# Optimization experiments

Measured on AMD Instinct MI355X. Metric: run time of the kernel, lower is better.

The kernel has to match this reference:

```python
import jax, jax.numpy as jnp
import numpy as np

E, D, P, T = 65536, 256, 4, 9
N_TYPES, N_SRC = 14, 4
# base-type order: nmos, pmos, balun, resistor, capacitor, inductor, vsource, isource, port
N_PARAMS = np.array([2, 2, 1, 1, 1, 1, 3, 2, 4], dtype=np.int32)
_S = np.ones((T, P), dtype=np.float32)
_S[0, 1] = 1e-6   # nmos w
_S[1, 1] = 1e-6   # pmos w
_S[3, 0] = 1e3    # resistor r
_S[4, 0] = 1e-12  # capacitor c
_S[5, 0] = 1e-9   # inductor l
_S[7, 0] = 1e-3   # isource dc
_S[7, 1] = 1e-3   # isource mag
_S[8, 2] = 1e9    # port freq
SCALES = jnp.asarray(_S)


def setup_inputs() -> dict:
    key = jax.random.key(0)
    ks = jax.random.split(key, 12)
    base_ids = jax.random.randint(ks[0], (E,), 0, T)
    type_ids = jax.random.randint(ks[1], (E,), 0, N_TYPES)
    source_ids = jax.random.randint(ks[2], (E,), 0, N_SRC)
    # raw params at physically realistic magnitude (pre-division values ~ scale)
    params = jax.random.uniform(ks[3], (E, P), jnp.float32) * SCALES[base_ids]
    W1 = jax.random.normal(ks[4], (T, P, D), jnp.float32) * 0.1
    # zero weight rows beyond each expert's param arity (matches torch pad/truncate)
    arity_mask = (np.arange(P)[None, :] < N_PARAMS[:, None]).astype(np.float32)
    W1 = W1 * jnp.asarray(arity_mask)[:, :, None]
    b1 = jax.random.normal(ks[5], (T, D), jnp.float32) * 0.1
    W2 = jax.random.normal(ks[6], (T, D, D), jnp.float32) * 0.05
    b2 = jax.random.normal(ks[7], (T, D), jnp.float32) * 0.05
    Wf = jax.random.normal(ks[8], (3 * D, D), jnp.float32) * 0.05
    bf = jax.random.normal(ks[9], (D,), jnp.float32) * 0.05
    type_embed = jax.random.normal(ks[10], (N_TYPES, D), jnp.float32)
    source_embed = jax.random.normal(ks[11], (N_SRC, D), jnp.float32)
    return {"type_ids": type_ids, "source_ids": source_ids, "base_ids": base_ids,
            "params": params, "type_embed": type_embed, "source_embed": source_embed,
            "W1": W1, "b1": b1, "W2": W2, "b2": b2, "Wf": Wf, "bf": bf}


def reference(type_ids, source_ids, base_ids, params, type_embed, source_embed,
              W1, b1, W2, b2, Wf, bf):
    # per-edge scale division (SCALE_FACTORS)
    x = params / SCALES[base_ids]                       # [E, P]
    # expert layer 1: gather tiny [P,D] weights per edge
    h = jax.nn.relu(jnp.einsum('ep,epd->ed', x, W1[base_ids]) + b1[base_ids])  # [E, D]
    # expert layer 2: masked per-type GEMMs (T is small/fixed)
    pv = jnp.zeros_like(h)
    for t in range(T):
        pv = jnp.where((base_ids == t)[:, None], h @ W2[t] + b2[t], pv)
    concat = jnp.concatenate([type_embed[type_ids], source_embed[source_ids], pv], axis=-1)  # [E, 3D]
    return jax.nn.relu(concat @ Wf + bf)                # [E, D]
```

## Files before the change

kernel.cpp:

```cpp
#include <hip/hip_runtime.h>

#define E_N 65536
#define T_N 9

typedef __bf16 bf16x8 __attribute__((ext_vector_type(8)));
typedef float f32x4 __attribute__((ext_vector_type(4)));
typedef unsigned short ushort8 __attribute__((ext_vector_type(8)));
union U8 { ushort8 u; bf16x8 b; };

#define OFF_CB   0
#define OFF_ABC  294912
#define OFF_D2   309248
#define OFF_BH   311552
#define OFF_CNT  313856
#define OFF_IDX  313872
#define WS_NEED_BYTES ((size_t)(313872 + 589824) * 4)

__device__ __constant__ float SCALES_C[9][4] = {
  {1.f,    1e-6f, 1.f,  1.f},
  {1.f,    1e-6f, 1.f,  1.f},
  {1.f,    1.f,   1.f,  1.f},
  {1e3f,   1.f,   1.f,  1.f},
  {1e-12f, 1.f,   1.f,  1.f},
  {1e-9f,  1.f,   1.f,  1.f},
  {1.f,    1.f,   1.f,  1.f},
  {1e-3f,  1e-3f, 1.f,  1.f},
  {1.f,    1.f,   1e9f, 1.f},
};

__device__ inline unsigned short f2bf(float f) {
  unsigned int u = __float_as_uint(f);
  unsigned int r = (u + 0x7FFFu + ((u >> 16) & 1u)) >> 16;
  return (unsigned short)r;
}

__global__ __launch_bounds__(256) void k_hist_embed(
    const int* __restrict__ base_ids,
    const float* __restrict__ te, const float* __restrict__ se,
    const float* __restrict__ b2, const float* __restrict__ Wf,
    const float* __restrict__ bfv,
    int* __restrict__ bh, float* __restrict__ ABc, float* __restrict__ D2b) {
  int b = blockIdx.x;
  int tid = threadIdx.x;

  if (b < 256) {
    __shared__ int ph[9][4];
    int e = (b << 8) + tid;
    int bt = base_ids[e];
    int w = tid >> 6, lane = tid & 63;
    #pragma unroll 1
    for (int t = 0; t < T_N; ++t) {
      unsigned long long m = __ballot(bt == t);
      if (lane == 0) ph[t][w] = __popcll(m);
    }
    __syncthreads();
    if (tid < T_N)
      bh[(tid << 8) + b] = ph[tid][0] + ph[tid][1] + ph[tid][2] + ph[tid][3];
  } else {
    int bb = b - 256, d = tid;
    if (bb < 56) {
      int ty = bb >> 2, sr = bb & 3;
      const float* t0 = te + ty * 256;
      const float* s0 = se + sr * 256;
      float a0 = 0.f, a1 = 0.f, a2 = 0.f, a3 = 0.f;
      #pragma unroll 4
      for (int k = 0; k < 256; k += 4) {
        a0 = fmaf(t0[k + 0], Wf[((k + 0) << 8) + d], a0);
        a1 = fmaf(t0[k + 1], Wf[((k + 1) << 8) + d], a1);
        a2 = fmaf(t0[k + 2], Wf[((k + 2) << 8) + d], a2);
        a3 = fmaf(t0[k + 3], Wf[((k + 3) << 8) + d], a3);
      }
      #pragma unroll 4
      for (int k = 0; k < 256; k += 4) {
        a0 = fmaf(s0[k + 0], Wf[((256 + k + 0) << 8) + d], a0);
        a1 = fmaf(s0[k + 1], Wf[((256 + k + 1) << 8) + d], a1);
        a2 = fmaf(s0[k + 2], Wf[((256 + k + 2) << 8) + d], a2);
        a3 = fmaf(s0[k + 3], Wf[((256 + k + 3) << 8) + d], a3);
      }
      ABc[(bb << 8) + d] = (a0 + a1) + (a2 + a3);
    } else {
      int t = bb - 56;
      const float* bp = b2 + t * 256;
      float a0 = bfv[d], a1 = 0.f, a2 = 0.f, a3 = 0.f;
      #pragma unroll 4
      for (int k = 0; k < 256; k += 4) {
        a0 = fmaf(bp[k + 0], Wf[((512 + k + 0) << 8) + d], a0);
        a1 = fmaf(bp[k + 1], Wf[((512 + k + 1) << 8) + d], a1);
        a2 = fmaf(bp[k + 2], Wf[((512 + k + 2) << 8) + d], a2);
        a3 = fmaf(bp[k + 3], Wf[((512 + k + 3) << 8) + d], a3);
      }
      D2b[(t << 8) + d] = (a0 + a1) + (a2 + a3);
    }
  }
}

__global__ __launch_bounds__(256) void k_c_scatter(
    const float* __restrict__ W2, const float* __restrict__ Wf,
    const int* __restrict__ base_ids, const int* __restrict__ type_ids,
    const int* __restrict__ source_ids, const int* __restrict__ bh,
    unsigned short* __restrict__ Cb, int* __restrict__ idx,
    int* __restrict__ cnt) {
  int b = blockIdx.x;
  int tid = threadIdx.x;

  if (b < 288) {
    int t = b >> 5;
    int j0 = (b & 31) << 3;
    __shared__ float w2s[8][256];
    for (int i = tid; i < 2048; i += 256)
      w2s[i >> 8][i & 255] = W2[t * 65536 + (j0 + (i >> 8)) * 256 + (i & 255)];
    __syncthreads();
    int dg = (tid & 63) << 2;
    int jg = (tid >> 6) << 1;
    f32x4 acc0 = {0.f, 0.f, 0.f, 0.f}, acc1 = {0.f, 0.f, 0.f, 0.f};
    #pragma unroll 4
    for (int k = 0; k < 256; ++k) {
      f32x4 wv = *(const f32x4*)&Wf[((512 + k) << 8) + dg];
      float a0 = w2s[jg][k], a1 = w2s[jg + 1][k];
      acc0.x = fmaf(a0, wv.x, acc0.x); acc0.y = fmaf(a0, wv.y, acc0.y);
      acc0.z = fmaf(a0, wv.z, acc0.z); acc0.w = fmaf(a0, wv.w, acc0.w);
      acc1.x = fmaf(a1, wv.x, acc1.x); acc1.y = fmaf(a1, wv.y, acc1.y);
      acc1.z = fmaf(a1, wv.z, acc1.z); acc1.w = fmaf(a1, wv.w, acc1.w);
    }
    unsigned short* CbT = Cb + (size_t)t * 65536;
    int j = j0 + jg;
    #pragma unroll
    for (int c = 0; c < 4; ++c) {
      int d = dg + c;
      unsigned int pk = (unsigned int)f2bf((c == 0) ? acc0.x : (c == 1) ? acc0.y : (c == 2) ? acc0.z : acc0.w)
                      | ((unsigned int)f2bf((c == 0) ? acc1.x : (c == 1) ? acc1.y : (c == 2) ? acc1.z : acc1.w) << 16);
      *(unsigned int*)&CbT[(((j >> 3) << 8) + d) * 8 + (j & 7)] = pk;
    }
  } else {
    int g = b - 288;
    int w = tid >> 6, lane = tid & 63;
    __shared__ int sph[9][4];
    __shared__ int redw[9][4];
    __shared__ int sbase[9];

    int e = (g << 8) + tid;
    int bt = base_ids[e];
    int pk = e | (type_ids[e] << 16) | (source_ids[e] << 20);
    unsigned long long lanebit = 1ull << lane;

    #pragma unroll 1
    for (int t = 0; t < T_N; ++t) {
      unsigned long long m = __ballot(bt == t);
      if (lane == 0) sph[t][w] = __popcll(m);
    }

    int v[9];
    #pragma unroll
    for (int t = 0; t < T_N; ++t) v[t] = (tid < g) ? bh[(t << 8) + tid] : 0;
    #pragma unroll
    for (int off = 32; off >= 1; off >>= 1) {
      #pragma unroll
      for (int t = 0; t < T_N; ++t) v[t] += __shfl_xor(v[t], off, 64);
    }
    if (lane == 0) {
      #pragma unroll
      for (int t = 0; t < T_N; ++t) redw[t][w] = v[t];
    }
    __syncthreads();
    if (tid < T_N) {
      sbase[tid] = redw[tid][0] + redw[tid][1] + redw[tid][2] + redw[tid][3];
      int tot = sph[tid][0] + sph[tid][1] + sph[tid][2] + sph[tid][3];
      if (g == 255) cnt[tid] = sbase[tid] + tot;
      int o = 0;
      #pragma unroll
      for (int ww = 0; ww < 4; ++ww) { int tmp = sph[tid][ww]; sph[tid][ww] = o; o += tmp; }
    }
    __syncthreads();

    #pragma unroll 1
    for (int t = 0; t < T_N; ++t) {
      unsigned long long m = __ballot(bt == t);
      if (bt == t) {
        int pos = sbase[t] + sph[t][w] + __popcll(m & (lanebit - 1ull));
        idx[t * E_N + pos] = pk;
      }
    }
  }
}

__global__ __launch_bounds__(256, 4) void edge_gemm(
    const int* __restrict__ cnt, const int* __restrict__ idxArr,
    const float* __restrict__ params,
    const float* __restrict__ W1, const float* __restrict__ b1,
    const unsigned short* __restrict__ Cb, const float* __restrict__ ABc,
    const float* __restrict__ D2b, float* __restrict__ out) {
  int b = blockIdx.x;
  int t = -1, m0 = 0, n = 0;
  {
    int acc = 0;
    #pragma unroll
    for (int tt = 0; tt < T_N; ++tt) {
      int c = cnt[tt];
      int nb = (c + 63) >> 6;
      if (t < 0 && b < acc + nb) { t = tt; m0 = (b - acc) << 6; n = c; }
      acc += nb;
    }
  }
  if (t < 0) return;

  __shared__ unsigned short hb[64 * 256];
  __shared__ int eidx[64];
  __shared__ float4 xs[64];

  int tid = threadIdx.x;
  if (tid < 64) {
    int m = m0 + tid;
    int mc = (m < n) ? m : (n - 1);
    int pk = idxArr[(size_t)t * E_N + mc];
    eidx[tid] = pk;
    int e = pk & 0xFFFF;
    float4 pr = *(const float4*)(params + (size_t)e * 4);
    float4 x;
    x.x = pr.x / SCALES_C[t][0];
    x.y = pr.y / SCALES_C[t][1];
    x.z = pr.z / SCALES_C[t][2];
    x.w = pr.w / SCALES_C[t][3];
    xs[tid] = x;
  }
  __syncthreads();

  {
    int d = tid;
    const float* W1t = W1 + t * 1024;
    float w0 = W1t[d], w1 = W1t[256 + d], w2 = W1t[512 + d], w3 = W1t[768 + d];
    float b1d = b1[t * 256 + d];
    int dbyte = d << 1;
    #pragma unroll 4
    for (int m = 0; m < 64; ++m) {
      float4 x = xs[m];
      float h = fmaf(x.x, w0, fmaf(x.y, w1, fmaf(x.z, w2, fmaf(x.w, w3, b1d))));
      h = fmaxf(h, 0.f);
      int off = (m << 9) + (dbyte ^ ((m & 7) << 4));
      hb[off >> 1] = f2bf(h);
    }
  }
  __syncthreads();

  int lane = tid & 63;
  int w = tid >> 6;
  int l15 = lane & 15;
  int l4 = lane >> 4;

  f32x4 acc[4][4];
  #pragma unroll
  for (int i = 0; i < 4; ++i)
    #pragma unroll
    for (int j = 0; j < 4; ++j) acc[i][j] = (f32x4){0.f, 0.f, 0.f, 0.f};

  const unsigned short* CbT = Cb + (size_t)t * 65536;

  #pragma unroll 1
  for (int s = 0; s < 8; ++s) {
    bf16x8 bfr[4];
    #pragma unroll
    for (int nn = 0; nn < 4; ++nn) {
      int koct = (s << 2) + l4;
      int d = (w << 6) + (nn << 4) + l15;
      U8 u;
      u.u = *(const ushort8*)(CbT + (size_t)((koct << 8) + d) * 8);
      bfr[nn] = u.b;
    }
    __builtin_amdgcn_s_setprio(1);
    #pragma unroll
    for (int mt = 0; mt < 4; ++mt) {
      int row = (mt << 4) + l15;
      int byte = (row << 9) + ((((s << 6) + (l4 << 4))) ^ ((row & 7) << 4));
      U8 a;
      a.u = *(const ushort8*)((const char*)hb + byte);
      #pragma unroll
      for (int nn = 0; nn < 4; ++nn)
        acc[mt][nn] = __builtin_amdgcn_mfma_f32_16x16x32_bf16(a.b, bfr[nn], acc[mt][nn], 0, 0, 0);
    }
    __builtin_amdgcn_s_setprio(0);
  }

  float* fb = (float*)hb;
  const float* d2p = D2b + (t << 8);
  #pragma unroll
  for (int p = 0; p < 2; ++p) {
    __syncthreads();
    #pragma unroll
    for (int mh = 0; mh < 2; ++mh) {
      int mt = (p << 1) + mh;
      int lrb = (mh << 4) + (l4 << 2);
      #pragma unroll
      for (int nn = 0; nn < 4; ++nn) {
        int col = (w << 6) + (nn << 4) + l15;
        #pragma unroll
        for (int r = 0; r < 4; ++r) {
          int lr = lrb + r;
          fb[lr * 256 + (col ^ ((lr & 7) << 2))] = acc[mt][nn][r];
        }
      }
    }
    __syncthreads();
    int lr = tid >> 3;
    int c8 = tid & 7;
    int row_g = (p << 5) + lr;
    if (m0 + row_g < n) {
      int pk = eidx[row_g];
      int e = pk & 0xFFFF;
      int ty = (pk >> 16) & 15;
      int sr = (pk >> 20) & 3;
      const float* abp = ABc + (size_t)(((ty << 2) + sr) << 8);
      float* op = out + (size_t)e * 256;
      int sw = (lr & 7) << 2;
      #pragma unroll
      for (int v = 0; v < 8; ++v) {
        int col = (c8 << 2) + (v << 5);
        f32x4 vv = *(const f32x4*)&fb[lr * 256 + (col ^ sw)];
        f32x4 ab = *(const f32x4*)&abp[col];
        f32x4 d2 = *(const f32x4*)&d2p[col];
        f32x4 rr;
        rr.x = fmaxf(vv.x + ab.x + d2.x, 0.f);
        rr.y = fmaxf(vv.y + ab.y + d2.y, 0.f);
        rr.z = fmaxf(vv.z + ab.z + d2.z, 0.f);
        rr.w = fmaxf(vv.w + ab.w + d2.w, 0.f);
        *(f32x4*)&op[col] = rr;
      }
    }
  }
}

extern "C" void kernel_launch(void* const* d_in, const int* in_sizes, int n_in,
                              void* d_out, int out_size, void* d_ws, size_t ws_size,
                              hipStream_t stream) {
  const int*   type_ids   = (const int*)  d_in[0];
  const int*   source_ids = (const int*)  d_in[1];
  const int*   base_ids   = (const int*)  d_in[2];
  const float* params     = (const float*)d_in[3];
  const float* type_embed = (const float*)d_in[4];
  const float* src_embed  = (const float*)d_in[5];
  const float* W1         = (const float*)d_in[6];
  const float* b1         = (const float*)d_in[7];
  const float* W2         = (const float*)d_in[8];
  const float* b2         = (const float*)d_in[9];
  const float* Wf         = (const float*)d_in[10];
  const float* bfv        = (const float*)d_in[11];
  float* out = (float*)d_out;

  if (ws_size < WS_NEED_BYTES) return;

  float* wsf = (float*)d_ws;
  unsigned short* Cb = (unsigned short*)(wsf + OFF_CB);
  float* ABc = wsf + OFF_ABC;
  float* D2b = wsf + OFF_D2;
  int*   bh  = (int*)(wsf + OFF_BH);
  int*   cnt = (int*)(wsf + OFF_CNT);
  int*   idx = (int*)(wsf + OFF_IDX);

  k_hist_embed<<<321, 256, 0, stream>>>(base_ids, type_embed, src_embed, b2, Wf,
                                        bfv, bh, ABc, D2b);
  k_c_scatter<<<544, 256, 0, stream>>>(W2, Wf, base_ids, type_ids, source_ids,
                                       bh, Cb, idx, cnt);
  edge_gemm<<<1033, 256, 0, stream>>>(cnt, idx, params, W1, b1, Cb, ABc, D2b, out);
}
```

Before: 66.37 us.

## Fuse prep and edge GEMM into one persistent cooperative kernel with grid sync

Replaces the three-kernel pipeline with a histogram kernel followed by one persistent cooperative kernel. That kernel runs the scatter, the embedding/bias projections and the W2·Wf product as work items in a grid-stride loop, then does a grid-wide sync and runs the edge GEMM tiles. Separately, the W2·Wf product is restructured so each block computes 8 rows with a K split across waves and an LDS reduction. The layer-1 h computation now processes two columns per thread with packed bf16 stores. The aim is to cut launch gaps and tail idle time between stages, at the cost of grid-sync overhead, more LDS through a union, and a persistent grid that may load-balance the GEMM tiles less well.

```diff
diff --git a/kernel.cpp b/kernel.cpp
--- a/kernel.cpp
+++ b/kernel.cpp
@@ -1,4 +1,7 @@
 #include <hip/hip_runtime.h>
+#include <hip/hip_cooperative_groups.h>
+
+namespace cg = cooperative_groups;
 
 #define E_N 65536
 #define T_N 9
@@ -7,6 +10,7 @@
 typedef float f32x4 __attribute__((ext_vector_type(4)));
 typedef unsigned short ushort8 __attribute__((ext_vector_type(8)));
 union U8 { ushort8 u; bf16x8 b; };
+union BF2 { __bf16 h[2]; unsigned int u; };
 
 #define OFF_CB   0
 #define OFF_ABC  294912
@@ -34,294 +38,344 @@
   return (unsigned short)r;
 }
 
-__global__ __launch_bounds__(256) void k_hist_embed(
-    const int* __restrict__ base_ids,
+struct GemmSM {
+  unsigned short hb[64 * 256];
+  int eidx[64];
+  float4 xs[64];
+};
+struct CSM {
+  float w2s[8][256];
+  float partf[3 * 64 * 32];
+};
+struct ScatSM {
+  int sph[9][4];
+  int redw[9][4];
+  int sbase[9];
+};
+union SM { GemmSM g; CSM c; ScatSM s; };
+
+__global__ __launch_bounds__(256) void k_hist(const int* __restrict__ base_ids,
+                                              int* __restrict__ bh) {
+  __shared__ int ph[9][4];
+  int b = blockIdx.x, tid = threadIdx.x;
+  int e = (b << 8) + tid;
+  int bt = base_ids[e];
+  int w = tid >> 6, lane = tid & 63;
+  #pragma unroll 1
+  for (int t = 0; t < T_N; ++t) {
+    unsigned long long m = __ballot(bt == t);
+    if (lane == 0) ph[t][w] = __popcll(m);
+  }
+  __syncthreads();
+  if (tid < T_N)
+    bh[(tid << 8) + b] = ph[tid][0] + ph[tid][1] + ph[tid][2] + ph[tid][3];
+}
+
+__global__ __launch_bounds__(256, 4) void fused(
+    int phase,
+    const int* __restrict__ base_ids, const int* __restrict__ type_ids,
+    const int* __restrict__ source_ids, const float* __restrict__ params,
     const float* __restrict__ te, const float* __restrict__ se,
-    const float* __restrict__ b2, const float* __restrict__ Wf,
-    const float* __restrict__ bfv,
-    int* __restrict__ bh, float* __restrict__ ABc, float* __restrict__ D2b) {
-  int b = blockIdx.x;
+    const float* __restrict__ W1, const float* __restrict__ b1,
+    const float* __restrict__ W2, const float* __restrict__ b2,
+    const float* __restrict__ Wf, const float* __restrict__ bfv,
+    const int* __restrict__ bh,
+    int* cnt, int* idxArr, unsigned short* Cb,
+    float* ABc, float* D2b, float* out) {
+  __shared__ SM sm;
   int tid = threadIdx.x;
-
-  if (b < 256) {
-    __shared__ int ph[9][4];
-    int e = (b << 8) + tid;
-    int bt = base_ids[e];
-    int w = tid >> 6, lane = tid & 63;
-    #pragma unroll 1
-    for (int t = 0; t < T_N; ++t) {
-      unsigned long long m = __ballot(bt == t);
-      if (lane == 0) ph[t][w] = __popcll(m);
-    }
-    __syncthreads();
-    if (tid < T_N)
-      bh[(tid << 8) + b] = ph[tid][0] + ph[tid][1] + ph[tid][2] + ph[tid][3];
-  } else {
-    int bb = b - 256, d = tid;
-    if (bb < 56) {
-      int ty = bb >> 2, sr = bb & 3;
-      const float* t0 = te + ty * 256;
-      const float* s0 = se + sr * 256;
-      float a0 = 0.f, a1 = 0.f, a2 = 0.f, a3 = 0.f;
-      #pragma unroll 4
-      for (int k = 0; k < 256; k += 4) {
-        a0 = fmaf(t0[k + 0], Wf[((k + 0) << 8) + d], a0);
-        a1 = fmaf(t0[k + 1], Wf[((k + 1) << 8) + d], a1);
-        a2 = fmaf(t0[k + 2], Wf[((k + 2) << 8) + d], a2);
-        a3 = fmaf(t0[k + 3], Wf[((k + 3) << 8) + d], a3);
-      }
-      #pragma unroll 4
-      for (int k = 0; k < 256; k += 4) {
-        a0 = fmaf(s0[k + 0], Wf[((256 + k + 0) << 8) + d], a0);
-        a1 = fmaf(s0[k + 1], Wf[((256 + k + 1) << 8) + d], a1);
-        a2 = fmaf(s0[k + 2], Wf[((256 + k + 2) << 8) + d], a2);
-        a3 = fmaf(s0[k + 3], Wf[((256 + k + 3) << 8) + d], a3);
-      }
-      ABc[(bb << 8) + d] = (a0 + a1) + (a2 + a3);
-    } else {
-      int t = bb - 56;
-      const float* bp = b2 + t * 256;
-      float a0 = bfv[d], a1 = 0.f, a2 = 0.f, a3 = 0.f;
-      #pragma unroll 4
-      for (int k = 0; k < 256; k += 4) {
-        a0 = fmaf(bp[k + 0], Wf[((512 + k + 0) << 8) + d], a0);
-        a1 = fmaf(bp[k + 1], Wf[((512 + k + 1) << 8) + d], a1);
-        a2 = fmaf(bp[k + 2], Wf[((512 + k + 2) << 8) + d], a2);
-        a3 = fmaf(bp[k + 3], Wf[((512 + k + 3) << 8) + d], a3);
-      }
-      D2b[(t << 8) + d] = (a0 + a1) + (a2 + a3);
-    }
-  }
-}
-
-__global__ __launch_bounds__(256) void k_c_scatter(
-    const float* __restrict__ W2, const float* __restrict__ Wf,
-    const int* __restrict__ base_ids, const int* __restrict__ type_ids,
-    const int* __restrict__ source_ids, const int* __restrict__ bh,
-    unsigned short* __restrict__ Cb, int* __restrict__ idx,
-    int* __restrict__ cnt) {
-  int b = blockIdx.x;
-  int tid = threadIdx.x;
-
-  if (b < 288) {
-    int t = b >> 5;
-    int j0 = (b & 31) << 3;
-    __shared__ float w2s[8][256];
-    for (int i = tid; i < 2048; i += 256)
-      w2s[i >> 8][i & 255] = W2[t * 65536 + (j0 + (i >> 8)) * 256 + (i & 255)];
-    __syncthreads();
-    int dg = (tid & 63) << 2;
-    int jg = (tid >> 6) << 1;
-    f32x4 acc0 = {0.f, 0.f, 0.f, 0.f}, acc1 = {0.f, 0.f, 0.f, 0.f};
-    #pragma unroll 4
-    for (int k = 0; k < 256; ++k) {
-      f32x4 wv = *(const f32x4*)&Wf[((512 + k) << 8) + dg];
-      float a0 = w2s[jg][k], a1 = w2s[jg + 1][k];
-      acc0.x = fmaf(a0, wv.x, acc0.x); acc0.y = fmaf(a0, wv.y, acc0.y);
-      acc0.z = fmaf(a0, wv.z, acc0.z); acc0.w = fmaf(a0, wv.w, acc0.w);
-      acc1.x = fmaf(a1, wv.x, acc1.x); acc1.y = fmaf(a1, wv.y, acc1.y);
-      acc1.z = fmaf(a1, wv.z, acc1.z); acc1.w = fmaf(a1, wv.w, acc1.w);
-    }
-    unsigned short* CbT = Cb + (size_t)t * 65536;
-    int j = j0 + jg;
-    #pragma unroll
-    for (int c = 0; c < 4; ++c) {
-      int d = dg + c;
-      unsigned int pk = (unsigned int)f2bf((c == 0) ? acc0.x : (c == 1) ? acc0.y : (c == 2) ? acc0.z : acc0.w)
-                      | ((unsigned int)f2bf((c == 0) ? acc1.x : (c == 1) ? acc1.y : (c == 2) ? acc1.z : acc1.w) << 16);
-      *(unsigned int*)&CbT[(((j >> 3) << 8) + d) * 8 + (j & 7)] = pk;
-    }
-  } else {
-    int g = b - 288;
-    int w = tid >> 6, lane = tid & 63;
-    __shared__ int sph[9][4];
-    __shared__ int redw[9][4];
-    __shared__ int sbase[9];
-
-    int e = (g << 8) + tid;
-    int bt = base_ids[e];
-    int pk = e | (type_ids[e] << 16) | (source_ids[e] << 20);
-    unsigned long long lanebit = 1ull << lane;
-
-    #pragma unroll 1
-    for (int t = 0; t < T_N; ++t) {
-      unsigned long long m = __ballot(bt == t);
-      if (lane == 0) sph[t][w] = __popcll(m);
-    }
-
-    int v[9];
-    #pragma unroll
-    for (int t = 0; t < T_N; ++t) v[t] = (tid < g) ? bh[(t << 8) + tid] : 0;
-    #pragma unroll
-    for (int off = 32; off >= 1; off >>= 1) {
-      #pragma unroll
-      for (int t = 0; t < T_N; ++t) v[t] += __shfl_xor(v[t], off, 64);
-    }
-    if (lane == 0) {
-      #pragma unroll
-      for (int t = 0; t < T_N; ++t) redw[t][w] = v[t];
-    }
-    __syncthreads();
-    if (tid < T_N) {
-      sbase[tid] = redw[tid][0] + redw[tid][1] + redw[tid][2] + redw[tid][3];
-      int tot = sph[tid][0] + sph[tid][1] + sph[tid][2] + sph[tid][3];
-      if (g == 255) cnt[tid] = sbase[tid] + tot;
-      int o = 0;
-      #pragma unroll
-      for (int ww = 0; ww < 4; ++ww) { int tmp = sph[tid][ww]; sph[tid][ww] = o; o += tmp; }
-    }
-    __syncthreads();
-
-    #pragma unroll 1
-    for (int t = 0; t < T_N; ++t) {
-      unsigned long long m = __ballot(bt == t);
-      if (bt == t) {
-        int pos = sbase[t] + sph[t][w] + __popcll(m & (lanebit - 1ull));
-        idx[t * E_N + pos] = pk;
-      }
-    }
-  }
-}
-
-__global__ __launch_bounds__(256, 4) void edge_gemm(
-    const int* __restrict__ cnt, const int* __restrict__ idxArr,
-    const float* __restrict__ params,
-    const float* __restrict__ W1, const float* __restrict__ b1,
-    const unsigned short* __restrict__ Cb, const float* __restrict__ ABc,
-    const float* __restrict__ D2b, float* __restrict__ out) {
-  int b = blockIdx.x;
-  int t = -1, m0 = 0, n = 0;
-  {
-    int acc = 0;
-    #pragma unroll
-    for (int tt = 0; tt < T_N; ++tt) {
-      int c = cnt[tt];
-      int nb = (c + 63) >> 6;
-      if (t < 0 && b < acc + nb) { t = tt; m0 = (b - acc) << 6; n = c; }
-      acc += nb;
-    }
-  }
-  if (t < 0) return;
-
-  __shared__ unsigned short hb[64 * 256];
-  __shared__ int eidx[64];
-  __shared__ float4 xs[64];
-
-  int tid = threadIdx.x;
-  if (tid < 64) {
-    int m = m0 + tid;
-    int mc = (m < n) ? m : (n - 1);
-    int pk = idxArr[(size_t)t * E_N + mc];
-    eidx[tid] = pk;
-    int e = pk & 0xFFFF;
-    float4 pr = *(const float4*)(params + (size_t)e * 4);
-    float4 x;
-    x.x = pr.x / SCALES_C[t][0];
-    x.y = pr.y / SCALES_C[t][1];
-    x.z = pr.z / SCALES_C[t][2];
-    x.w = pr.w / SCALES_C[t][3];
-    xs[tid] = x;
-  }
-  __syncthreads();
-
-  {
-    int d = tid;
-    const float* W1t = W1 + t * 1024;
-    float w0 = W1t[d], w1 = W1t[256 + d], w2 = W1t[512 + d], w3 = W1t[768 + d];
-    float b1d = b1[t * 256 + d];
-    int dbyte = d << 1;
-    #pragma unroll 4
-    for (int m = 0; m < 64; ++m) {
-      float4 x = xs[m];
-      float h = fmaf(x.x, w0, fmaf(x.y, w1, fmaf(x.z, w2, fmaf(x.w, w3, b1d))));
-      h = fmaxf(h, 0.f);
-      int off = (m << 9) + (dbyte ^ ((m & 7) << 4));
-      hb[off >> 1] = f2bf(h);
-    }
-  }
-  __syncthreads();
-
+  int nb = gridDim.x;
   int lane = tid & 63;
   int w = tid >> 6;
-  int l15 = lane & 15;
-  int l4 = lane >> 4;
-
-  f32x4 acc[4][4];
-  #pragma unroll
-  for (int i = 0; i < 4; ++i)
+
+  if (phase <= 1) {
+    for (int it = blockIdx.x; it < 609; it += nb) {
+      if (it < 256) {
+        int g = it;
+        int e = (g << 8) + tid;
+        int bt = base_ids[e];
+        int pk = e | (type_ids[e] << 16) | (source_ids[e] << 20);
+        unsigned long long lanebit = 1ull << lane;
+
+        #pragma unroll 1
+        for (int t = 0; t < T_N; ++t) {
+          unsigned long long m = __ballot(bt == t);
+          if (lane == 0) sm.s.sph[t][w] = __popcll(m);
+        }
+        int v[9];
+        #pragma unroll
+        for (int t = 0; t < T_N; ++t) v[t] = (tid < g) ? bh[(t << 8) + tid] : 0;
+        #pragma unroll
+        for (int off = 32; off >= 1; off >>= 1) {
+          #pragma unroll
+          for (int t = 0; t < T_N; ++t) v[t] += __shfl_xor(v[t], off, 64);
+        }
+        if (lane == 0) {
+          #pragma unroll
+          for (int t = 0; t < T_N; ++t) sm.s.redw[t][w] = v[t];
+        }
+        __syncthreads();
+        if (tid < T_N) {
+          sm.s.sbase[tid] = sm.s.redw[tid][0] + sm.s.redw[tid][1] +
+                            sm.s.redw[tid][2] + sm.s.redw[tid][3];
+          int tot = sm.s.sph[tid][0] + sm.s.sph[tid][1] +
+                    sm.s.sph[tid][2] + sm.s.sph[tid][3];
+          if (g == 255) cnt[tid] = sm.s.sbase[tid] + tot;
+          int o = 0;
+          #pragma unroll
+          for (int ww = 0; ww < 4; ++ww) {
+            int tmp = sm.s.sph[tid][ww]; sm.s.sph[tid][ww] = o; o += tmp;
+          }
+        }
+        __syncthreads();
+        #pragma unroll 1
+        for (int t = 0; t < T_N; ++t) {
+          unsigned long long m = __ballot(bt == t);
+          if (bt == t) {
+            int pos = sm.s.sbase[t] + sm.s.sph[t][w] + __popcll(m & (lanebit - 1ull));
+            idxArr[t * E_N + pos] = pk;
+          }
+        }
+      } else if (it < 321) {
+        int bb = it - 256, d = tid;
+        if (bb < 56) {
+          int ty = bb >> 2, sr = bb & 3;
+          const float* t0 = te + ty * 256;
+          const float* s0 = se + sr * 256;
+          float a0 = 0.f, a1 = 0.f, a2 = 0.f, a3 = 0.f;
+          #pragma unroll 4
+          for (int k = 0; k < 256; k += 4) {
+            a0 = fmaf(t0[k + 0], Wf[((k + 0) << 8) + d], a0);
+            a1 = fmaf(t0[k + 1], Wf[((k + 1) << 8) + d], a1);
+            a2 = fmaf(t0[k + 2], Wf[((k + 2) << 8) + d], a2);
+            a3 = fmaf(t0[k + 3], Wf[((k + 3) << 8) + d], a3);
+          }
+          #pragma unroll 4
+          for (int k = 0; k < 256; k += 4) {
+            a0 = fmaf(s0[k + 0], Wf[((256 + k + 0) << 8) + d], a0);
+            a1 = fmaf(s0[k + 1], Wf[((256 + k + 1) << 8) + d], a1);
+            a2 = fmaf(s0[k + 2], Wf[((256 + k + 2) << 8) + d], a2);
+            a3 = fmaf(s0[k + 3], Wf[((256 + k + 3) << 8) + d], a3);
+          }
+          ABc[(bb << 8) + d] = (a0 + a1) + (a2 + a3);
+        } else {
+          int t = bb - 56;
+          const float* bp = b2 + t * 256;
+          float a0 = bfv[d], a1 = 0.f, a2 = 0.f, a3 = 0.f;
+          #pragma unroll 4
+          for (int k = 0; k < 256; k += 4) {
+            a0 = fmaf(bp[k + 0], Wf[((512 + k + 0) << 8) + d], a0);
+            a1 = fmaf(bp[k + 1], Wf[((512 + k + 1) << 8) + d], a1);
+            a2 = fmaf(bp[k + 2], Wf[((512 + k + 2) << 8) + d], a2);
+            a3 = fmaf(bp[k + 3], Wf[((512 + k + 3) << 8) + d], a3);
+          }
+          D2b[(t << 8) + d] = (a0 + a1) + (a2 + a3);
+        }
+      } else {
+        int ci = it - 321;
+        int t = ci >> 5;
+        int j0 = (ci & 31) << 3;
+        for (int i = tid; i < 2048; i += 256)
+          sm.c.w2s[i >> 8][i & 255] =
+              W2[(size_t)t * 65536 + (size_t)(j0 + (i >> 8)) * 256 + (i & 255)];
+        __syncthreads();
+
+        int dg = lane << 2;
+        int kbase = w << 6;
+        f32x4 acc[8];
+        #pragma unroll
+        for (int j = 0; j < 8; ++j) acc[j] = (f32x4){0.f, 0.f, 0.f, 0.f};
+        #pragma unroll 2
+        for (int k0 = 0; k0 < 64; k0 += 4) {
+          f32x4 a[8];
+          #pragma unroll
+          for (int j = 0; j < 8; ++j) a[j] = *(const f32x4*)&sm.c.w2s[j][kbase + k0];
+          #pragma unroll
+          for (int kk = 0; kk < 4; ++kk) {
+            f32x4 wv = *(const f32x4*)&Wf[((512 + kbase + k0 + kk) << 8) + dg];
+            #pragma unroll
+            for (int j = 0; j < 8; ++j) {
+              float aj = a[j][kk];
+              acc[j].x = fmaf(aj, wv.x, acc[j].x);
+              acc[j].y = fmaf(aj, wv.y, acc[j].y);
+              acc[j].z = fmaf(aj, wv.z, acc[j].z);
+              acc[j].w = fmaf(aj, wv.w, acc[j].w);
+            }
+          }
+        }
+        if (w > 0) {
+          int fb = (((w - 1) << 6) + lane) << 5;
+          #pragma unroll
+          for (int j = 0; j < 8; ++j)
+            *(f32x4*)&sm.c.partf[fb + ((j ^ (lane & 7)) << 2)] = acc[j];
+        }
+        __syncthreads();
+        if (w == 0) {
+          #pragma unroll
+          for (int p = 0; p < 3; ++p) {
+            int fb = ((p << 6) + lane) << 5;
+            #pragma unroll
+            for (int j = 0; j < 8; ++j)
+              acc[j] += *(const f32x4*)&sm.c.partf[fb + ((j ^ (lane & 7)) << 2)];
+          }
+          unsigned short* CbT = Cb + (size_t)t * 65536;
+          #pragma unroll
+          for (int di = 0; di < 4; ++di) {
+            ushort8 o;
+            #pragma unroll
+            for (int j = 0; j < 8; ++j) o[j] = f2bf(acc[j][di]);
+            *(ushort8*)(CbT + ((size_t)((j0 >> 3) << 8) + dg + di) * 8) = o;
+          }
+        }
+      }
+      __syncthreads();
+    }
+  }
+
+  if (phase < 0) {
+    __threadfence();
+    cg::this_grid().sync();
+  }
+
+  if (phase < 0 || phase == 2) {
+    int tcnt[9];
     #pragma unroll
-    for (int j = 0; j < 4; ++j) acc[i][j] = (f32x4){0.f, 0.f, 0.f, 0.f};
-
-  const unsigned short* CbT = Cb + (size_t)t * 65536;
-
-  #pragma unroll 1
-  for (int s = 0; s < 8; ++s) {
-    bf16x8 bfr[4];
+    for (int i2 = 0; i2 < 9; ++i2) tcnt[i2] = cnt[i2];
+    int tot = 0;
     #pragma unroll
-    for (int nn = 0; nn < 4; ++nn) {
-      int koct = (s << 2) + l4;
-      int d = (w << 6) + (nn << 4) + l15;
-      U8 u;
-      u.u = *(const ushort8*)(CbT + (size_t)((koct << 8) + d) * 8);
-      bfr[nn] = u.b;
-    }
-    __builtin_amdgcn_s_setprio(1);
-    #pragma unroll
-    for (int mt = 0; mt < 4; ++mt) {
-      int row = (mt << 4) + l15;
-      int byte = (row << 9) + ((((s << 6) + (l4 << 4))) ^ ((row & 7) << 4));
-      U8 a;
-      a.u = *(const ushort8*)((const char*)hb + byte);
+    for (int i2 = 0; i2 < 9; ++i2) tot += (tcnt[i2] + 63) >> 6;
+
+    for (int tile = blockIdx.x; tile < tot; tile += nb) {
+      __syncthreads();
+      int t = 0, m0 = 0, accb = 0;
       #pragma unroll
-      for (int nn = 0; nn < 4; ++nn)
-        acc[mt][nn] = __builtin_amdgcn_mfma_f32_16x16x32_bf16(a.b, bfr[nn], acc[mt][nn], 0, 0, 0);
-    }
-    __builtin_amdgcn_s_setprio(0);
-  }
-
-  float* fb = (float*)hb;
-  const float* d2p = D2b + (t << 8);
-  #pragma unroll
-  for (int p = 0; p < 2; ++p) {
-    __syncthreads();
-    #pragma unroll
-    for (int mh = 0; mh < 2; ++mh) {
-      int mt = (p << 1) + mh;
-      int lrb = (mh << 4) + (l4 << 2);
+      for (int tt = 0; tt < T_N; ++tt) {
+        int nbk = (tcnt[tt] + 63) >> 6;
+        if (tile >= accb && tile < accb + nbk) { t = tt; m0 = (tile - accb) << 6; }
+        accb += nbk;
+      }
+      int n = tcnt[t];
+
+      if (tid < 64) {
+        int m = m0 + tid;
+        int mc = (m < n) ? m : (n - 1);
+        int pk = idxArr[(size_t)t * E_N + mc];
+        sm.g.eidx[tid] = pk;
+        int e = pk & 0xFFFF;
+        float4 pr = *(const float4*)(params + (size_t)e * 4);
+        float4 x;
+        x.x = pr.x / SCALES_C[t][0];
+        x.y = pr.y / SCALES_C[t][1];
+        x.z = pr.z / SCALES_C[t][2];
+        x.w = pr.w / SCALES_C[t][3];
+        sm.g.xs[tid] = x;
+      }
+      __syncthreads();
+
+      {
+        int dp = tid & 127, mh = tid >> 7;
+        int d0 = dp << 1;
+        const float* W1t = W1 + t * 1024;
+        float2 wq0 = *(const float2*)&W1t[d0];
+        float2 wq1 = *(const float2*)&W1t[256 + d0];
+        float2 wq2 = *(const float2*)&W1t[512 + d0];
+        float2 wq3 = *(const float2*)&W1t[768 + d0];
+        float2 bq  = *(const float2*)&b1[t * 256 + d0];
+        int mb = mh << 5;
+        #pragma unroll 4
+        for (int i = 0; i < 32; ++i) {
+          int m = mb + i;
+          float4 x = sm.g.xs[m];
+          float h0 = fmaf(x.x, wq0.x, fmaf(x.y, wq1.x, fmaf(x.z, wq2.x, fmaf(x.w, wq3.x, bq.x))));
+          float h1 = fmaf(x.x, wq0.y, fmaf(x.y, wq1.y, fmaf(x.z, wq2.y, fmaf(x.w, wq3.y, bq.y))));
+          BF2 pk2;
+          pk2.h[0] = (__bf16)fmaxf(h0, 0.f);
+          pk2.h[1] = (__bf16)fmaxf(h1, 0.f);
+          int off = (m << 9) + ((d0 << 1) ^ ((m & 7) << 4));
+          *(unsigned int*)((char*)sm.g.hb + off) = pk2.u;
+        }
+      }
+      __syncthreads();
+
+      int l15 = lane & 15;
+      int l4 = lane >> 4;
+      f32x4 acc[4][4];
       #pragma unroll
-      for (int nn = 0; nn < 4; ++nn) {
-        int col = (w << 6) + (nn << 4) + l15;
-        #pragma unroll
-        for (int r = 0; r < 4; ++r) {
-          int lr = lrb + r;
-          fb[lr * 256 + (col ^ ((lr & 7) << 2))] = acc[mt][nn][r];
-        }
-      }
-    }
-    __syncthreads();
-    int lr = tid >> 3;
-    int c8 = tid & 7;
-    int row_g = (p << 5) + lr;
-    if (m0 + row_g < n) {
-      int pk = eidx[row_g];
-      int e = pk & 0xFFFF;
-      int ty = (pk >> 16) & 15;
-      int sr = (pk >> 20) & 3;
-      const float* abp = ABc + (size_t)(((ty << 2) + sr) << 8);
-      float* op = out + (size_t)e * 256;
-      int sw = (lr & 7) << 2;
+      for (int i = 0; i < 4; ++i)
+        #pragma unroll
+        for (int j = 0; j < 4; ++j) acc[i][j] = (f32x4){0.f, 0.f, 0.f, 0.f};
+
+      const unsigned short* CbT = Cb + (size_t)t * 65536;
+      #pragma unroll 1
+      for (int s = 0; s < 8; ++s) {
+        bf16x8 bfr[4];
+        #pragma unroll
+        for (int nn = 0; nn < 4; ++nn) {
+          int koct = (s << 2) + l4;
+          int d = (w << 6) + (nn << 4) + l15;
+          U8 u;
+          u.u = *(const ushort8*)(CbT + (size_t)((koct << 8) + d) * 8);
+          bfr[nn] = u.b;
+        }
+        __builtin_amdgcn_s_setprio(1);
+        #pragma unroll
+        for (int mt = 0; mt < 4; ++mt) {
+          int row = (mt << 4) + l15;
+          int byte = (row << 9) + ((((s << 6) + (l4 << 4))) ^ ((row & 7) << 4));
+          U8 a;
+          a.u = *(const ushort8*)((const char*)sm.g.hb + byte);
+          #pragma unroll
+          for (int nn = 0; nn < 4; ++nn)
+            acc[mt][nn] = __builtin_amdgcn_mfma_f32_16x16x32_bf16(a.b, bfr[nn], acc[mt][nn], 0, 0, 0);
+        }
+        __builtin_amdgcn_s_setprio(0);
+      }
+
+      float* fb = (float*)sm.g.hb;
+      const float* d2p = D2b + (t << 8);
       #pragma unroll
-      for (int v = 0; v < 8; ++v) {
-        int col = (c8 << 2) + (v << 5);
-        f32x4 vv = *(const f32x4*)&fb[lr * 256 + (col ^ sw)];
-        f32x4 ab = *(const f32x4*)&abp[col];
-        f32x4 d2 = *(const f32x4*)&d2p[col];
-        f32x4 rr;
-        rr.x = fmaxf(vv.x + ab.x + d2.x, 0.f);
-        rr.y = fmaxf(vv.y + ab.y + d2.y, 0.f);
-        rr.z = fmaxf(vv.z + ab.z + d2.z, 0.f);
-        rr.w = fmaxf(vv.w + ab.w + d2.w, 0.f);
-        *(f32x4*)&op[col] = rr;
+      for (int p = 0; p < 2; ++p) {
+        __syncthreads();
+        #pragma unroll
+        for (int mh2 = 0; mh2 < 2; ++mh2) {
+          int mt = (p << 1) + mh2;
+          int lrb = (mh2 << 4) + (l4 << 2);
+          #pragma unroll
+          for (int nn = 0; nn < 4; ++nn) {
+            int col = (w << 6) + (nn << 4) + l15;
+            #pragma unroll
+            for (int r = 0; r < 4; ++r) {
+              int lr = lrb + r;
+              fb[lr * 256 + (col ^ ((lr & 7) << 2))] = acc[mt][nn][r];
+            }
+          }
+        }
+        __syncthreads();
+        int lr = tid >> 3;
+        int c8 = tid & 7;
+        int row_g = (p << 5) + lr;
+        if (m0 + row_g < n) {
+          int pk = sm.g.eidx[row_g];
+          int e = pk & 0xFFFF;
+          int ty = (pk >> 16) & 15;
+          int sr = (pk >> 20) & 3;
+          const float* abp = ABc + (size_t)(((ty << 2) + sr) << 8);
+          float* op = out + (size_t)e * 256;
+          int sw = (lr & 7) << 2;
+          #pragma unroll
+          for (int vv2 = 0; vv2 < 8; ++vv2) {
+            int col = (c8 << 2) + (vv2 << 5);
+            f32x4 vvv = *(const f32x4*)&fb[lr * 256 + (col ^ sw)];
+            f32x4 ab = *(const f32x4*)&abp[col];
+            f32x4 d2 = *(const f32x4*)&d2p[col];
+            f32x4 rr;
+            rr.x = fmaxf(vvv.x + ab.x + d2.x, 0.f);
+            rr.y = fmaxf(vvv.y + ab.y + d2.y, 0.f);
+            rr.z = fmaxf(vvv.z + ab.z + d2.z, 0.f);
+            rr.w = fmaxf(vvv.w + ab.w + d2.w, 0.f);
+            *(f32x4*)&op[col] = rr;
+          }
+        }
       }
     }
   }
@@ -334,8 +388,8 @@
   const int*   source_ids = (const int*)  d_in[1];
   const int*   base_ids   = (const int*)  d_in[2];
   const float* params     = (const float*)d_in[3];
-  const float* type_embed = (const float*)d_in[4];
-  const float* src_embed  = (const float*)d_in[5];
+  const float* te         = (const float*)d_in[4];
+  const float* se         = (const float*)d_in[5];
   const float* W1         = (const float*)d_in[6];
   const float* b1         = (const float*)d_in[7];
   const float* W2         = (const float*)d_in[8];
@@ -354,9 +408,35 @@
   int*   cnt = (int*)(wsf + OFF_CNT);
   int*   idx = (int*)(wsf + OFF_IDX);
 
-  k_hist_embed<<<321, 256, 0, stream>>>(base_ids, type_embed, src_embed, b2, Wf,
-                                        bfv, bh, ABc, D2b);
-  k_c_scatter<<<544, 256, 0, stream>>>(W2, Wf, base_ids, type_ids, source_ids,
-                                       bh, Cb, idx, cnt);
-  edge_gemm<<<1033, 256, 0, stream>>>(cnt, idx, params, W1, b1, Cb, ABc, D2b, out);
+  k_hist<<<256, 256, 0, stream>>>(base_ids, bh);
+
+  int maxb = 0;
+  hipError_t oe = hipOccupancyMaxActiveBlocksPerMultiprocessor(
+      &maxb, (const void*)fused, 256, 0);
+  int grid = (oe == hipSuccess && maxb > 0) ? maxb * 256 : 0;
+  if (grid > 1024) grid = 1024;
+  bool coop = (grid >= 256);
+
+  if (coop) {
+    int ph = -1;
+    void* args[] = {(void*)&ph,
+                    (void*)&base_ids, (void*)&type_ids, (void*)&source_ids,
+                    (void*)&params,   (void*)&te,       (void*)&se,
+                    (void*)&W1,       (void*)&b1,       (void*)&W2,
+                    (void*)&b2,       (void*)&Wf,       (void*)&bfv,
+                    (void*)&bh,       (void*)&cnt,      (void*)&idx,
+                    (void*)&Cb,       (void*)&ABc,      (void*)&D2b,
+                    (void*)&out};
+    hipError_t le = hipLaunchCooperativeKernel((const void*)fused, dim3(grid),
+                                               dim3(256), args, 0, stream);
+    if (le != hipSuccess) coop = false;
+  }
+  if (!coop) {
+    fused<<<609, 256, 0, stream>>>(1, base_ids, type_ids, source_ids, params,
+                                   te, se, W1, b1, W2, b2, Wf, bfv, bh, cnt,
+                                   idx, Cb, ABc, D2b, out);
+    fused<<<1033, 256, 0, stream>>>(2, base_ids, type_ids, source_ids, params,
+                                    te, se, W1, b1, W2, b2, Wf, bfv, bh, cnt,
+                                    idx, Cb, ABc, D2b, out);
+  }
 }
```

Result: slower. 198.2 us (+198.6%).

## Fuse histogram, scatter and weight precompute into one prep kernel using atomics

Applied to the files above, without the earlier changes.

Merges the two preprocessing kernels into a single launch. Each block now claims its bucket offset with an atomicAdd on a per-type counter instead of the two-pass histogram plus prefix sum, and the counter is zeroed with a memset. The embedding and C-matrix precompute blocks are rewritten to split K across the four waves with vectorized float4 loads and a shared-memory reduction, and C now packs 8 outputs per store. This removes a kernel launch and the serial dependency on the histogram. The cost is that edge order within each type bucket is no longer deterministic, plus an extra memset node.

```diff
diff --git a/kernel.cpp b/kernel.cpp
--- a/kernel.cpp
+++ b/kernel.cpp
@@ -11,10 +11,9 @@
 #define OFF_CB   0
 #define OFF_ABC  294912
 #define OFF_D2   309248
-#define OFF_BH   311552
-#define OFF_CNT  313856
-#define OFF_IDX  313872
-#define WS_NEED_BYTES ((size_t)(313872 + 589824) * 4)
+#define OFF_CNT  311552
+#define OFF_IDX  311568
+#define WS_NEED_BYTES ((size_t)(311568 + 589824) * 4)
 
 __device__ __constant__ float SCALES_C[9][4] = {
   {1.f,    1e-6f, 1.f,  1.f},
@@ -34,150 +33,156 @@
   return (unsigned short)r;
 }
 
-__global__ __launch_bounds__(256) void k_hist_embed(
-    const int* __restrict__ base_ids,
+struct ScatSM { int sph[9][4]; int sbase[9]; };
+struct EmbSM  { float partf[4 * 64 * 4]; };
+struct CSM    { float w2s[8][256]; float partf[3 * 8 * 64 * 4]; };
+union PrepSM  { ScatSM s; EmbSM e; CSM c; };
+
+__global__ __launch_bounds__(256) void k_prep(
+    const int* __restrict__ base_ids, const int* __restrict__ type_ids,
+    const int* __restrict__ source_ids,
     const float* __restrict__ te, const float* __restrict__ se,
     const float* __restrict__ b2, const float* __restrict__ Wf,
-    const float* __restrict__ bfv,
-    int* __restrict__ bh, float* __restrict__ ABc, float* __restrict__ D2b) {
+    const float* __restrict__ bfv, const float* __restrict__ W2,
+    int* __restrict__ cnt, int* __restrict__ idxArr,
+    unsigned short* __restrict__ Cb,
+    float* __restrict__ ABc, float* __restrict__ D2b) {
+  __shared__ PrepSM sm;
   int b = blockIdx.x;
   int tid = threadIdx.x;
+  int lane = tid & 63;
+  int w = tid >> 6;
 
   if (b < 256) {
-    __shared__ int ph[9][4];
     int e = (b << 8) + tid;
     int bt = base_ids[e];
-    int w = tid >> 6, lane = tid & 63;
+    int pk = e | (type_ids[e] << 16) | (source_ids[e] << 20);
+    unsigned long long lanebit = 1ull << lane;
+
     #pragma unroll 1
     for (int t = 0; t < T_N; ++t) {
       unsigned long long m = __ballot(bt == t);
-      if (lane == 0) ph[t][w] = __popcll(m);
-    }
-    __syncthreads();
-    if (tid < T_N)
-      bh[(tid << 8) + b] = ph[tid][0] + ph[tid][1] + ph[tid][2] + ph[tid][3];
-  } else {
-    int bb = b - 256, d = tid;
-    if (bb < 56) {
-      int ty = bb >> 2, sr = bb & 3;
-      const float* t0 = te + ty * 256;
-      const float* s0 = se + sr * 256;
-      float a0 = 0.f, a1 = 0.f, a2 = 0.f, a3 = 0.f;
-      #pragma unroll 4
-      for (int k = 0; k < 256; k += 4) {
-        a0 = fmaf(t0[k + 0], Wf[((k + 0) << 8) + d], a0);
-        a1 = fmaf(t0[k + 1], Wf[((k + 1) << 8) + d], a1);
-        a2 = fmaf(t0[k + 2], Wf[((k + 2) << 8) + d], a2);
-        a3 = fmaf(t0[k + 3], Wf[((k + 3) << 8) + d], a3);
-      }
-      #pragma unroll 4
-      for (int k = 0; k < 256; k += 4) {
-        a0 = fmaf(s0[k + 0], Wf[((256 + k + 0) << 8) + d], a0);
-        a1 = fmaf(s0[k + 1], Wf[((256 + k + 1) << 8) + d], a1);
-        a2 = fmaf(s0[k + 2], Wf[((256 + k + 2) << 8) + d], a2);
-        a3 = fmaf(s0[k + 3], Wf[((256 + k + 3) << 8) + d], a3);
-      }
-      ABc[(bb << 8) + d] = (a0 + a1) + (a2 + a3);
-    } else {
-      int t = bb - 56;
-      const float* bp = b2 + t * 256;
-      float a0 = bfv[d], a1 = 0.f, a2 = 0.f, a3 = 0.f;
-      #pragma unroll 4
-      for (int k = 0; k < 256; k += 4) {
-        a0 = fmaf(bp[k + 0], Wf[((512 + k + 0) << 8) + d], a0);
-        a1 = fmaf(bp[k + 1], Wf[((512 + k + 1) << 8) + d], a1);
-        a2 = fmaf(bp[k + 2], Wf[((512 + k + 2) << 8) + d], a2);
-        a3 = fmaf(bp[k + 3], Wf[((512 + k + 3) << 8) + d], a3);
-      }
-      D2b[(t << 8) + d] = (a0 + a1) + (a2 + a3);
-    }
-  }
-}
-
-__global__ __launch_bounds__(256) void k_c_scatter(
-    const float* __restrict__ W2, const float* __restrict__ Wf,
-    const int* __restrict__ base_ids, const int* __restrict__ type_ids,
-    const int* __restrict__ source_ids, const int* __restrict__ bh,
-    unsigned short* __restrict__ Cb, int* __restrict__ idx,
-    int* __restrict__ cnt) {
-  int b = blockIdx.x;
-  int tid = threadIdx.x;
-
-  if (b < 288) {
-    int t = b >> 5;
-    int j0 = (b & 31) << 3;
-    __shared__ float w2s[8][256];
-    for (int i = tid; i < 2048; i += 256)
-      w2s[i >> 8][i & 255] = W2[t * 65536 + (j0 + (i >> 8)) * 256 + (i & 255)];
-    __syncthreads();
-    int dg = (tid & 63) << 2;
-    int jg = (tid >> 6) << 1;
-    f32x4 acc0 = {0.f, 0.f, 0.f, 0.f}, acc1 = {0.f, 0.f, 0.f, 0.f};
-    #pragma unroll 4
-    for (int k = 0; k < 256; ++k) {
-      f32x4 wv = *(const f32x4*)&Wf[((512 + k) << 8) + dg];
-      float a0 = w2s[jg][k], a1 = w2s[jg + 1][k];
-      acc0.x = fmaf(a0, wv.x, acc0.x); acc0.y = fmaf(a0, wv.y, acc0.y);
-      acc0.z = fmaf(a0, wv.z, acc0.z); acc0.w = fmaf(a0, wv.w, acc0.w);
-      acc1.x = fmaf(a1, wv.x, acc1.x); acc1.y = fmaf(a1, wv.y, acc1.y);
-      acc1.z = fmaf(a1, wv.z, acc1.z); acc1.w = fmaf(a1, wv.w, acc1.w);
-    }
-    unsigned short* CbT = Cb + (size_t)t * 65536;
-    int j = j0 + jg;
-    #pragma unroll
-    for (int c = 0; c < 4; ++c) {
-      int d = dg + c;
-      unsigned int pk = (unsigned int)f2bf((c == 0) ? acc0.x : (c == 1) ? acc0.y : (c == 2) ? acc0.z : acc0.w)
-                      | ((unsigned int)f2bf((c == 0) ? acc1.x : (c == 1) ? acc1.y : (c == 2) ? acc1.z : acc1.w) << 16);
-      *(unsigned int*)&CbT[(((j >> 3) << 8) + d) * 8 + (j & 7)] = pk;
-    }
-  } else {
-    int g = b - 288;
-    int w = tid >> 6, lane = tid & 63;
-    __shared__ int sph[9][4];
-    __shared__ int redw[9][4];
-    __shared__ int sbase[9];
-
-    int e = (g << 8) + tid;
-    int bt = base_ids[e];
-    int pk = e | (type_ids[e] << 16) | (source_ids[e] << 20);
-    unsigned long long lanebit = 1ull << lane;
-
-    #pragma unroll 1
-    for (int t = 0; t < T_N; ++t) {
-      unsigned long long m = __ballot(bt == t);
-      if (lane == 0) sph[t][w] = __popcll(m);
-    }
-
-    int v[9];
-    #pragma unroll
-    for (int t = 0; t < T_N; ++t) v[t] = (tid < g) ? bh[(t << 8) + tid] : 0;
-    #pragma unroll
-    for (int off = 32; off >= 1; off >>= 1) {
-      #pragma unroll
-      for (int t = 0; t < T_N; ++t) v[t] += __shfl_xor(v[t], off, 64);
-    }
-    if (lane == 0) {
-      #pragma unroll
-      for (int t = 0; t < T_N; ++t) redw[t][w] = v[t];
+      if (lane == 0) sm.s.sph[t][w] = __popcll(m);
     }
     __syncthreads();
     if (tid < T_N) {
-      sbase[tid] = redw[tid][0] + redw[tid][1] + redw[tid][2] + redw[tid][3];
-      int tot = sph[tid][0] + sph[tid][1] + sph[tid][2] + sph[tid][3];
-      if (g == 255) cnt[tid] = sbase[tid] + tot;
-      int o = 0;
-      #pragma unroll
-      for (int ww = 0; ww < 4; ++ww) { int tmp = sph[tid][ww]; sph[tid][ww] = o; o += tmp; }
-    }
-    __syncthreads();
-
+      int c0 = sm.s.sph[tid][0], c1 = sm.s.sph[tid][1];
+      int c2 = sm.s.sph[tid][2], c3 = sm.s.sph[tid][3];
+      int tot = c0 + c1 + c2 + c3;
+      int base = (tot > 0) ? atomicAdd(&cnt[tid], tot) : 0;
+      sm.s.sbase[tid] = base;
+      sm.s.sph[tid][0] = 0;
+      sm.s.sph[tid][1] = c0;
+      sm.s.sph[tid][2] = c0 + c1;
+      sm.s.sph[tid][3] = c0 + c1 + c2;
+    }
+    __syncthreads();
     #pragma unroll 1
     for (int t = 0; t < T_N; ++t) {
       unsigned long long m = __ballot(bt == t);
       if (bt == t) {
-        int pos = sbase[t] + sph[t][w] + __popcll(m & (lanebit - 1ull));
-        idx[t * E_N + pos] = pk;
+        int pos = sm.s.sbase[t] + sm.s.sph[t][w] + __popcll(m & (lanebit - 1ull));
+        idxArr[t * E_N + pos] = pk;
+      }
+    }
+  } else if (b < 321) {
+    int bb = b - 256;
+    int dg = lane << 2;
+    f32x4 acc0 = {0.f, 0.f, 0.f, 0.f}, acc1 = {0.f, 0.f, 0.f, 0.f};
+    if (bb < 56) {
+      int ty = bb >> 2, sr = bb & 3;
+      const float* src = (w < 2) ? (te + ty * 256) : (se + sr * 256 - 256);
+      int kbase = w << 7;
+      #pragma unroll 8
+      for (int k = kbase; k < kbase + 128; k += 2) {
+        f32x4 wv0 = *(const f32x4*)&Wf[((k + 0) << 8) + dg];
+        f32x4 wv1 = *(const f32x4*)&Wf[((k + 1) << 8) + dg];
+        float e0 = src[k], e1 = src[k + 1];
+        acc0.x = fmaf(e0, wv0.x, acc0.x); acc0.y = fmaf(e0, wv0.y, acc0.y);
+        acc0.z = fmaf(e0, wv0.z, acc0.z); acc0.w = fmaf(e0, wv0.w, acc0.w);
+        acc1.x = fmaf(e1, wv1.x, acc1.x); acc1.y = fmaf(e1, wv1.y, acc1.y);
+        acc1.z = fmaf(e1, wv1.z, acc1.z); acc1.w = fmaf(e1, wv1.w, acc1.w);
+      }
+    } else {
+      int t = bb - 56;
+      const float* bp = b2 + t * 256;
+      int kbase = w << 6;
+      #pragma unroll 8
+      for (int k = kbase; k < kbase + 64; k += 2) {
+        f32x4 wv0 = *(const f32x4*)&Wf[((512 + k + 0) << 8) + dg];
+        f32x4 wv1 = *(const f32x4*)&Wf[((512 + k + 1) << 8) + dg];
+        float e0 = bp[k], e1 = bp[k + 1];
+        acc0.x = fmaf(e0, wv0.x, acc0.x); acc0.y = fmaf(e0, wv0.y, acc0.y);
+        acc0.z = fmaf(e0, wv0.z, acc0.z); acc0.w = fmaf(e0, wv0.w, acc0.w);
+        acc1.x = fmaf(e1, wv1.x, acc1.x); acc1.y = fmaf(e1, wv1.y, acc1.y);
+        acc1.z = fmaf(e1, wv1.z, acc1.z); acc1.w = fmaf(e1, wv1.w, acc1.w);
+      }
+    }
+    acc0 += acc1;
+    *(f32x4*)&sm.e.partf[((w << 6) + lane) << 2] = acc0;
+    __syncthreads();
+    if (w == 0) {
+      acc0 += *(const f32x4*)&sm.e.partf[((1 << 6) + lane) << 2];
+      acc0 += *(const f32x4*)&sm.e.partf[((2 << 6) + lane) << 2];
+      acc0 += *(const f32x4*)&sm.e.partf[((3 << 6) + lane) << 2];
+      if (bb < 56) {
+        *(f32x4*)&ABc[(bb << 8) + dg] = acc0;
+      } else {
+        f32x4 bv = *(const f32x4*)&bfv[dg];
+        *(f32x4*)&D2b[((bb - 56) << 8) + dg] = acc0 + bv;
+      }
+    }
+  } else {
+    int ci = b - 321;
+    int t = ci >> 5;
+    int j0 = (ci & 31) << 3;
+    for (int i = tid; i < 2048; i += 256)
+      sm.c.w2s[i >> 8][i & 255] =
+          W2[(size_t)t * 65536 + (size_t)(j0 + (i >> 8)) * 256 + (i & 255)];
+    __syncthreads();
+
+    int dg = lane << 2;
+    int kbase = w << 6;
+    f32x4 acc[8];
+    #pragma unroll
+    for (int j = 0; j < 8; ++j) acc[j] = (f32x4){0.f, 0.f, 0.f, 0.f};
+    #pragma unroll 2
+    for (int k0 = 0; k0 < 64; k0 += 4) {
+      f32x4 a[8];
+      #pragma unroll
+      for (int j = 0; j < 8; ++j) a[j] = *(const f32x4*)&sm.c.w2s[j][kbase + k0];
+      #pragma unroll
+      for (int kk = 0; kk < 4; ++kk) {
+        f32x4 wv = *(const f32x4*)&Wf[((512 + kbase + k0 + kk) << 8) + dg];
+        #pragma unroll
+        for (int j = 0; j < 8; ++j) {
+          float aj = a[j][kk];
+          acc[j].x = fmaf(aj, wv.x, acc[j].x);
+          acc[j].y = fmaf(aj, wv.y, acc[j].y);
+          acc[j].z = fmaf(aj, wv.z, acc[j].z);
+          acc[j].w = fmaf(aj, wv.w, acc[j].w);
+        }
+      }
+    }
+    if (w > 0) {
+      #pragma unroll
+      for (int j = 0; j < 8; ++j)
+        *(f32x4*)&sm.c.partf[(((((w - 1) << 3) + j) << 6) + lane) << 2] = acc[j];
+    }
+    __syncthreads();
+    if (w == 0) {
+      #pragma unroll
+      for (int p = 0; p < 3; ++p)
+        #pragma unroll
+        for (int j = 0; j < 8; ++j)
+          acc[j] += *(const f32x4*)&sm.c.partf[((((p << 3) + j) << 6) + lane) << 2];
+      unsigned short* CbT = Cb + (size_t)t * 65536;
+      #pragma unroll
+      for (int di = 0; di < 4; ++di) {
+        ushort8 o;
+        #pragma unroll
+        for (int j = 0; j < 8; ++j) o[j] = f2bf(acc[j][di]);
+        *(ushort8*)(CbT + ((size_t)((j0 >> 3) << 8) + dg + di) * 8) = o;
       }
     }
   }
@@ -334,8 +339,8 @@
   const int*   source_ids = (const int*)  d_in[1];
   const int*   base_ids   = (const int*)  d_in[2];
   const float* params     = (const float*)d_in[3];
-  const float* type_embed = (const float*)d_in[4];
-  const float* src_embed  = (const float*)d_in[5];
+  const float* te         = (const float*)d_in[4];
+  const float* se         = (const float*)d_in[5];
   const float* W1         = (const float*)d_in[6];
   const float* b1         = (const float*)d_in[7];
   const float* W2         = (const float*)d_in[8];
@@ -350,13 +355,11 @@
   unsigned short* Cb = (unsigned short*)(wsf + OFF_CB);
   float* ABc = wsf + OFF_ABC;
   float* D2b = wsf + OFF_D2;
-  int*   bh  = (int*)(wsf + OFF_BH);
   int*   cnt = (int*)(wsf + OFF_CNT);
   int*   idx = (int*)(wsf + OFF_IDX);
 
-  k_hist_embed<<<321, 256, 0, stream>>>(base_ids, type_embed, src_embed, b2, Wf,
-                                        bfv, bh, ABc, D2b);
-  k_c_scatter<<<544, 256, 0, stream>>>(W2, Wf, base_ids, type_ids, source_ids,
-                                       bh, Cb, idx, cnt);
+  hipMemsetAsync(cnt, 0, 16 * sizeof(int), stream);
+  k_prep<<<609, 256, 0, stream>>>(base_ids, type_ids, source_ids, te, se, b2,
+                                  Wf, bfv, W2, cnt, idx, Cb, ABc, D2b);
   edge_gemm<<<1033, 256, 0, stream>>>(cnt, idx, params, W1, b1, Cb, ABc, D2b, out);
 }
```

Result: faster. 58.97 us (-11.1%).
